# Optimization experiments

Hardware: AMD Instinct MI355X
Metric: run time of the kernel (lower is better)

The kernel has to match this reference:

```python
import jax, jax.numpy as jnp
import numpy as np

N_HEAD = 12
SCALING = 0.17677669529663687  # 1/sqrt(head_dim=32)


def setup_inputs() -> dict:
    key = jax.random.key(0)
    ks = jax.random.split(key, 6)
    B, R, C, E = 1, 256, 384, 384
    s = 1.0 / np.sqrt(E)
    return {
        "x": jax.random.normal(ks[0], (B, R, C, E), dtype=jnp.float32),
        "Wq": (jax.random.normal(ks[1], (E, E), dtype=jnp.float32) * s),
        "Wk": (jax.random.normal(ks[2], (E, E), dtype=jnp.float32) * s),
        "Wv": (jax.random.normal(ks[3], (E, E), dtype=jnp.float32) * s),
        "Wq_s": (jax.random.normal(ks[4], (E, E), dtype=jnp.float32) * s),
        "Wk_s": (jax.random.normal(ks[5], (E, E), dtype=jnp.float32) * s),
        "res_mask": jnp.ones((B, C), dtype=jnp.int32),
        "seq_mask": jnp.ones((B, R), dtype=jnp.int32),
    }


def reference(x, Wq, Wk, Wv, Wq_s, Wk_s, res_mask, seq_mask):
    B, R, C, E = x.shape
    H = N_HEAD
    D = E // H
    NEG = jnp.finfo(x.dtype).min

    # ---- SeqWeightAttention: per-column attention over rows, query = row 0 ----
    scale_s = 1.0 / np.sqrt(D)
    msa = jnp.transpose(x, (0, 2, 1, 3))                 # [B,C,R,E]
    q0 = msa[:, :, 0]                                    # [B,C,E]
    Qs = (q0 @ Wq_s).reshape(B, C, 1, H, D)
    Qs = jnp.transpose(Qs, (0, 1, 3, 2, 4)) * scale_s    # [B,C,H,1,D]
    Ks = (msa @ Wk_s).reshape(B, C, R, H, D)
    Ks = jnp.transpose(Ks, (0, 1, 3, 4, 2))              # [B,C,H,D,R]
    QKs = Qs @ Ks                                        # [B,C,H,1,R]
    QKs = jnp.where(seq_mask[:, None, None, None, :] == 0, NEG, QKs)
    sw = jax.nn.softmax(QKs, axis=-1)
    sw = jnp.transpose(sw, (0, 4, 1, 2, 3))              # [B,R,C,H,1]

    # ---- main attention, row-contracted (attn_seq_weight path) ----
    scaling = SCALING / np.sqrt(C)                        # seqlen_scaling=True
    Q = (x @ Wq).reshape(B, R, C, H, D) * scaling * sw    # Q modulated by seq weights
    K = (x @ Wk).reshape(B, R, C, H, D)
    V = (x @ Wv).reshape(B, R, C, H, D)

    QK = jnp.einsum('brihd,brjhd->bhij', Q, K)            # contract rows + head_dim
    rm = res_mask[:, :, None] * res_mask[:, None, :]      # [B,C,C]
    QK = jnp.where(rm[:, None, :, :] == 0, NEG, QK)
    attn = jax.nn.softmax(QK, axis=-1)                    # [B,H,C,C]

    out = jnp.einsum('bhij,brjhd->brihd', attn, V)
    return out.reshape(B, R, C, E)
```

## Files before the change

### kernel.cpp

```cpp
#include <hip/hip_runtime.h>
#include <math.h>
#include <stdint.h>

#define DEV_INLINE __device__ __forceinline__

constexpr int R_ = 256, C_ = 384, E_ = 384, H_ = 12, D_ = 32;
constexpr float NEGF = -3.402823466e38f;

typedef __attribute__((ext_vector_type(4))) float f32x4;
typedef __attribute__((ext_vector_type(8))) short short8;
typedef __attribute__((ext_vector_type(4))) unsigned short u16x4;

constexpr size_t o_qs     = 0;
constexpr size_t o_p      = o_qs + (size_t)C_ * E_;
constexpr size_t o_logits = o_p + (size_t)C_ * H_ * E_;
constexpr size_t o_sw     = o_logits + (size_t)C_ * H_ * R_;
constexpr size_t o_attn   = o_sw + (size_t)C_ * H_ * R_;
constexpr size_t o_q3     = o_attn + (size_t)H_ * C_ * C_;
constexpr size_t SZBIG  = 75497472;
constexpr size_t ob_q3b = o_q3 * 4;
constexpr size_t ob_k3b = ob_q3b + SZBIG;
constexpr size_t ob_v3b = ob_k3b + SZBIG;
constexpr size_t ob_xb  = ob_v3b + SZBIG;

DEV_INLINE unsigned short bf16h(float x) {
  unsigned int u = __builtin_bit_cast(unsigned int, x);
  unsigned int r = (u + 0x7FFFu + ((u >> 16) & 1u)) >> 16;
  return (unsigned short)r;
}
DEV_INLINE float waveRedMax(float v) {
#pragma unroll
  for (int o = 32; o > 0; o >>= 1) v = fmaxf(v, __shfl_down(v, o));
  return v;
}
DEV_INLINE float waveRedSum(float v) {
#pragma unroll
  for (int o = 32; o > 0; o >>= 1) v += __shfl_down(v, o);
  return v;
}

DEV_INLINE void gll16(const void* g, void* l) {
  __builtin_amdgcn_global_load_lds(
      reinterpret_cast<__attribute__((address_space(1))) void*>(
          reinterpret_cast<uintptr_t>(g)),
      reinterpret_cast<__attribute__((address_space(3))) void*>(
          reinterpret_cast<uintptr_t>(l)),
      16, 0, 0);
}

template <int ROWS, int UPR, int MASK, int SHIFT>
DEV_INLINE void stageT(const unsigned short* __restrict__ g, int lda,
                       unsigned short* l) {
  int t = threadIdx.x, w = t >> 6, lane = t & 63;
  constexpr int NI = (ROWS * UPR) / 64;
  constexpr int PW = NI / 4;
#pragma unroll
  for (int j = 0; j < PW; ++j) {
    int u0 = (w * PW + j) * 64;
    int u = u0 + lane;
    int row = u / UPR, qp = u % UPR;
    int q = qp ^ ((row >> SHIFT) & MASK);
    gll16(g + (size_t)row * lda + q * 8, l + (size_t)u0 * 8);
  }
}

template <int MASK, int SHIFT>
DEV_INLINE short8 fragLd(const unsigned short* base, int row, int q, int rowShorts) {
  int qp = q ^ ((row >> SHIFT) & MASK);
  return *(const short8*)(base + row * rowShorts + qp * 8);
}

__global__ void k_qs(const float* __restrict__ x, const float* __restrict__ Wq_s,
                     float* __restrict__ ws) {
  int c = blockIdx.x, t = threadIdx.x;
  __shared__ float xl[E_];
  xl[t] = x[(size_t)c * E_ + t];
  __syncthreads();
  float s = 0.f;
#pragma unroll 8
  for (int k = 0; k < E_; ++k) s += xl[k] * Wq_s[(size_t)k * E_ + t];
  ws[o_qs + (size_t)c * E_ + t] = s * 0.17677669529663687f;
}

__global__ void k_p(const float* __restrict__ Wk_s, const float* __restrict__ ws,
                    unsigned short* __restrict__ Pb) {
  int h = blockIdx.x, c = blockIdx.y, t = threadIdx.x;
  __shared__ float q[D_];
  float s = 0.f;
  if (h < 12) {
    if (t < D_) q[t] = ws[o_qs + (size_t)c * E_ + h * D_ + t];
    __syncthreads();
    const float* wrow = &Wk_s[(size_t)t * E_ + h * D_];
#pragma unroll
    for (int d = 0; d < D_; d += 4) {
      float4 w = *(const float4*)&wrow[d];
      s += w.x * q[d] + w.y * q[d + 1] + w.z * q[d + 2] + w.w * q[d + 3];
    }
  }
  Pb[((size_t)c * 16 + h) * 384 + t] = bf16h(s);
}

__global__ __launch_bounds__(256) void k_logits_sm(
    const unsigned short* __restrict__ xb, const unsigned short* __restrict__ Pb,
    const int* __restrict__ seq_mask, float* __restrict__ swT) {
  int c = blockIdx.x, t = threadIdx.x;
  __shared__ unsigned short sA[256 * 32];
  __shared__ unsigned short sB[16 * 32];
  __shared__ float lg[12 * 256];
  __shared__ float red[4];
  int w = t >> 6, lane = t & 63, id16 = lane & 15, g = lane >> 4;
  f32x4 acc[4];
#pragma unroll
  for (int mi = 0; mi < 4; ++mi) acc[mi] = (f32x4){0.f, 0.f, 0.f, 0.f};

  for (int k0 = 0; k0 < 384; k0 += 32) {
    stageT<256, 4, 3, 0>(xb + (size_t)c * 384 + k0, 384 * 384, sA);
    if (w == 0) {
      int row = lane >> 2, qp = lane & 3, q = qp ^ (row & 3);
      gll16(Pb + ((size_t)c * 16 + row) * 384 + k0 + q * 8, sB);
    }
    __syncthreads();
    short8 Bf = fragLd<3, 0>(sB, id16, g, 32);
#pragma unroll
    for (int mi = 0; mi < 4; ++mi) {
      short8 Af = fragLd<3, 0>(sA, w * 64 + mi * 16 + id16, g, 32);
      acc[mi] = __builtin_amdgcn_mfma_f32_16x16x32_bf16(Af, Bf, acc[mi], 0, 0, 0);
    }
    __syncthreads();
  }
  int l4 = (lane >> 4) * 4;
#pragma unroll
  for (int mi = 0; mi < 4; ++mi) {
    if (id16 < 12) {
      f32x4 a = acc[mi];
#pragma unroll
      for (int reg = 0; reg < 4; ++reg)
        lg[id16 * 256 + w * 64 + mi * 16 + l4 + reg] = a[reg];
    }
  }
  __syncthreads();
  int wid = t >> 6;
  const float scal = 0.17677669529663687f / sqrtf((float)C_);
  bool masked = (seq_mask[t] == 0);
  for (int h = 0; h < 12; ++h) {
    float v = masked ? NEGF : lg[h * 256 + t];
    float m = waveRedMax(v);
    if ((t & 63) == 0) red[wid] = m;
    __syncthreads();
    float mx = fmaxf(fmaxf(red[0], red[1]), fmaxf(red[2], red[3]));
    __syncthreads();
    float e = expf(v - mx);
    float s = waveRedSum(e);
    if ((t & 63) == 0) red[wid] = s;
    __syncthreads();
    float sum = red[0] + red[1] + red[2] + red[3];
    swT[((size_t)h * 256 + t) * 384 + c] = e / sum * scal;
    __syncthreads();
  }
}

__global__ void k_cvt_x(const float* __restrict__ x, unsigned short* __restrict__ xb) {
  size_t i = ((size_t)blockIdx.x * 256 + threadIdx.x) * 16;
  unsigned short h[16];
#pragma unroll
  for (int j = 0; j < 4; ++j) {
    float4 f = *(const float4*)&x[i + j * 4];
    h[j * 4 + 0] = bf16h(f.x);
    h[j * 4 + 1] = bf16h(f.y);
    h[j * 4 + 2] = bf16h(f.z);
    h[j * 4 + 3] = bf16h(f.w);
  }
  *(short8*)&xb[i] = *(const short8*)&h[0];
  *(short8*)&xb[i + 8] = *(const short8*)&h[8];
}

__global__ void k_cvt_w(const float* __restrict__ Wq, const float* __restrict__ Wk,
                        const float* __restrict__ Wv, unsigned short* __restrict__ Wtb) {
  int n = blockIdx.x, k = threadIdx.x;
  const float* W;
  int col;
  if (n < 384)      { W = Wq; col = n; }
  else if (n < 768) { W = Wk; col = n - 384; }
  else              { W = Wv; col = n - 768; }
  Wtb[(size_t)n * 384 + k] = bf16h(W[(size_t)k * 384 + col]);
}

__global__ __launch_bounds__(256, 4) void k_proj_all(
    const unsigned short* __restrict__ xb, const unsigned short* __restrict__ Wtb,
    const float* __restrict__ swT, unsigned short* __restrict__ Q3b,
    unsigned short* __restrict__ K3b, unsigned short* __restrict__ V3b) {
  __shared__ unsigned short smem[2 * 128 * 64];
  unsigned short* sA = smem;
  unsigned short* sB = smem + 128 * 64;
  int Dd = blockIdx.x;
  int L = (Dd & 7) * 864 + (Dd >> 3);
  int bm = L / 9, bn = L - bm * 9;
  int n0 = bn * 128, m0 = bm * 128;
  int wave = threadIdx.x >> 6, wr = wave >> 1, wc = wave & 1;
  int lane = threadIdx.x & 63, id16 = lane & 15, g = lane >> 4;
  f32x4 acc[4][4];
#pragma unroll
  for (int mi = 0; mi < 4; ++mi)
#pragma unroll
    for (int ni = 0; ni < 4; ++ni) acc[mi][ni] = (f32x4){0.f, 0.f, 0.f, 0.f};

  for (int it = 0; it < 6; ++it) {
    stageT<128, 8, 7, 0>(xb + (size_t)m0 * 384 + it * 64, 384, sA);
    stageT<128, 8, 7, 0>(Wtb + (size_t)n0 * 384 + it * 64, 384, sB);
    __syncthreads();
    short8 Af[4][2], Bf[4][2];
#pragma unroll
    for (int mi = 0; mi < 4; ++mi) {
      int row = wr * 64 + mi * 16 + id16;
#pragma unroll
      for (int kk = 0; kk < 2; ++kk) Af[mi][kk] = fragLd<7, 0>(sA, row, kk * 4 + g, 64);
    }
#pragma unroll
    for (int ni = 0; ni < 4; ++ni) {
      int col = wc * 64 + ni * 16 + id16;
#pragma unroll
      for (int kk = 0; kk < 2; ++kk) Bf[ni][kk] = fragLd<7, 0>(sB, col, kk * 4 + g, 64);
    }
#pragma unroll
    for (int kk = 0; kk < 2; ++kk)
#pragma unroll
      for (int mi = 0; mi < 4; ++mi)
#pragma unroll
        for (int ni = 0; ni < 4; ++ni)
          acc[mi][ni] = __builtin_amdgcn_mfma_f32_16x16x32_bf16(Af[mi][kk], Bf[ni][kk],
                                                                acc[mi][ni], 0, 0, 0);
    __syncthreads();
  }

  int l4 = (lane >> 4) * 4;
  int r = bm / 3, cb = (bm % 3) * 128;
  if (bn < 6) {
    bool isQ = bn < 3;
    int hbase = isQ ? bn * 4 : (bn - 3) * 4;
#pragma unroll
    for (int mi = 0; mi < 4; ++mi) {
      int clBase = wr * 64 + mi * 16 + l4;
#pragma unroll
      for (int ni = 0; ni < 4; ++ni) {
        int nl = wc * 64 + ni * 16 + id16;
        int hhl = nl >> 5, d = nl & 31;
        f32x4 a = acc[mi][ni];
        if (isQ) {
          float4 sv =
              *(const float4*)&swT[((size_t)(hbase + hhl) * 256 + r) * 384 + cb + clBase];
          a[0] *= sv.x; a[1] *= sv.y; a[2] *= sv.z; a[3] *= sv.w;
        }
#pragma unroll
        for (int reg = 0; reg < 4; ++reg)
          smem[hhl * 4096 + (clBase + reg) * 32 + d] = bf16h(a[reg]);
      }
    }
    __syncthreads();
    unsigned short* dst = isQ ? Q3b : K3b;
#pragma unroll
    for (int seg = 0; seg < 8; ++seg) {
      int off = seg * 2048 + threadIdx.x * 8;
      int hhl = off >> 12, inner = off & 4095;
      int hg = hbase + hhl;
      *(short8*)(dst + (((size_t)hg * 256 + r) * 384 + cb) * 32 + inner) =
          *(const short8*)(smem + off);
    }
  } else {
    int r2 = r, cb2 = cb;
#pragma unroll
    for (int mi = 0; mi < 4; ++mi) {
      int c0 = cb2 + wr * 64 + mi * 16 + l4;
#pragma unroll
      for (int ni = 0; ni < 4; ++ni) {
        int nv = n0 + wc * 64 + ni * 16 + id16 - 768;
        int hh = nv >> 5, dd = nv & 31;
        f32x4 a = acc[mi][ni];
        u16x4 hv;
#pragma unroll
        for (int reg = 0; reg < 4; ++reg) hv[reg] = bf16h(a[reg]);
        *(u16x4*)(V3b + ((size_t)hh * 8192 + r2 * 32 + dd) * 384 + c0) = hv;
      }
    }
  }
}

__global__ __launch_bounds__(256, 4) void k_qk_mma(
    const unsigned short* __restrict__ Q3b, const unsigned short* __restrict__ K3b,
    float* __restrict__ QKf0, float* __restrict__ QKf1) {
  __shared__ unsigned short sA[2 * 4096], sB[2 * 4096];
  int Dd = blockIdx.x;
  int L = (Dd & 7) * 27 + (Dd >> 3);
  int kh = L / 108, rem = L - kh * 108;
  int h = rem / 9, r2 = rem - h * 9, bi = r2 / 3, bj = r2 - bi * 3;
  int i0 = bi * 128, j0 = bj * 128;
  int wave = threadIdx.x >> 6, wr = wave >> 1, wc = wave & 1;
  int lane = threadIdx.x & 63, id16 = lane & 15, g = lane >> 4;
  f32x4 acc[4][4];
#pragma unroll
  for (int mi = 0; mi < 4; ++mi)
#pragma unroll
    for (int ni = 0; ni < 4; ++ni) acc[mi][ni] = (f32x4){0.f, 0.f, 0.f, 0.f};

  for (int it = 0; it < 64; ++it) {
    int r = kh * 128 + it * 2;
#pragma unroll
    for (int rr = 0; rr < 2; ++rr) {
      stageT<128, 4, 3, 1>(Q3b + (((size_t)h * 256 + r + rr) * 384 + i0) * 32, 32,
                           sA + rr * 4096);
      stageT<128, 4, 3, 1>(K3b + (((size_t)h * 256 + r + rr) * 384 + j0) * 32, 32,
                           sB + rr * 4096);
    }
    __syncthreads();
#pragma unroll
    for (int rr = 0; rr < 2; ++rr) {
      short8 Af[4], Bf[4];
#pragma unroll
      for (int mi = 0; mi < 4; ++mi)
        Af[mi] = fragLd<3, 1>(sA + rr * 4096, wr * 64 + mi * 16 + id16, g, 32);
#pragma unroll
      for (int ni = 0; ni < 4; ++ni)
        Bf[ni] = fragLd<3, 1>(sB + rr * 4096, wc * 64 + ni * 16 + id16, g, 32);
#pragma unroll
      for (int mi = 0; mi < 4; ++mi)
#pragma unroll
        for (int ni = 0; ni < 4; ++ni)
          acc[mi][ni] = __builtin_amdgcn_mfma_f32_16x16x32_bf16(Af[mi], Bf[ni],
                                                                acc[mi][ni], 0, 0, 0);
    }
    __syncthreads();
  }
  int l4 = (lane >> 4) * 4;
  float* dst = kh ? QKf1 : QKf0;
#pragma unroll
  for (int mi = 0; mi < 4; ++mi)
#pragma unroll
    for (int ni = 0; ni < 4; ++ni) {
      int ii = i0 + wr * 64 + mi * 16 + l4;
      int j = j0 + wc * 64 + ni * 16 + id16;
      f32x4 a = acc[mi][ni];
#pragma unroll
      for (int reg = 0; reg < 4; ++reg)
        dst[((size_t)h * 384 + ii + reg) * 384 + j] = a[reg];
    }
}

__global__ void k_softmax_j(const int* __restrict__ res_mask, const float* __restrict__ QKf0,
                            const float* __restrict__ QKf1,
                            unsigned short* __restrict__ attnb) {
  int i = blockIdx.x, h = blockIdx.y, t = threadIdx.x;
  int lane = t & 63, wid = t >> 6;
  size_t base = ((size_t)h * C_ + i) * C_;
  float v = QKf0[base + t] + QKf1[base + t];
  if ((res_mask[i] * res_mask[t]) == 0) v = NEGF;
  __shared__ float red[6];
  float m = waveRedMax(v);
  if (lane == 0) red[wid] = m;
  __syncthreads();
  float mx = red[0];
#pragma unroll
  for (int w = 1; w < 6; ++w) mx = fmaxf(mx, red[w]);
  __syncthreads();
  float e = expf(v - mx);
  float s = waveRedSum(e);
  if (lane == 0) red[wid] = s;
  __syncthreads();
  float sum = 0.f;
#pragma unroll
  for (int w = 0; w < 6; ++w) sum += red[w];
  attnb[base + t] = bf16h(e / sum);
}

__global__ __launch_bounds__(256, 4) void k_out_mma(
    const unsigned short* __restrict__ attnb, const unsigned short* __restrict__ V3b,
    float* __restrict__ out) {
  __shared__ unsigned short sA[128 * 64], sB[128 * 64];
  int Dd = blockIdx.x;
  int L = (Dd & 7) * 288 + (Dd >> 3);
  int bn = L % 64, bm = (L / 64) % 3, h = L / 192;
  int n0 = bn * 128, m0 = bm * 128;
  int wave = threadIdx.x >> 6, wr = wave >> 1, wc = wave & 1;
  int lane = threadIdx.x & 63, id16 = lane & 15, g = lane >> 4;
  f32x4 acc[4][4];
#pragma unroll
  for (int mi = 0; mi < 4; ++mi)
#pragma unroll
    for (int ni = 0; ni < 4; ++ni) acc[mi][ni] = (f32x4){0.f, 0.f, 0.f, 0.f};
  const unsigned short* Ab = attnb + (size_t)h * 384 * 384 + (size_t)m0 * 384;
  const unsigned short* Bb = V3b + (size_t)h * 8192 * 384 + (size_t)n0 * 384;

  for (int it = 0; it < 6; ++it) {
    stageT<128, 8, 7, 0>(Ab + it * 64, 384, sA);
    stageT<128, 8, 7, 0>(Bb + it * 64, 384, sB);
    __syncthreads();
    short8 Af[4][2], Bf[4][2];
#pragma unroll
    for (int mi = 0; mi < 4; ++mi) {
      int row = wr * 64 + mi * 16 + id16;
#pragma unroll
      for (int kk = 0; kk < 2; ++kk) Af[mi][kk] = fragLd<7, 0>(sA, row, kk * 4 + g, 64);
    }
#pragma unroll
    for (int ni = 0; ni < 4; ++ni) {
      int col = wc * 64 + ni * 16 + id16;
#pragma unroll
      for (int kk = 0; kk < 2; ++kk) Bf[ni][kk] = fragLd<7, 0>(sB, col, kk * 4 + g, 64);
    }
#pragma unroll
    for (int kk = 0; kk < 2; ++kk)
#pragma unroll
      for (int mi = 0; mi < 4; ++mi)
#pragma unroll
        for (int ni = 0; ni < 4; ++ni)
          acc[mi][ni] = __builtin_amdgcn_mfma_f32_16x16x32_bf16(Af[mi][kk], Bf[ni][kk],
                                                                acc[mi][ni], 0, 0, 0);
    __syncthreads();
  }
  int l4 = (lane >> 4) * 4;
#pragma unroll
  for (int mi = 0; mi < 4; ++mi)
#pragma unroll
    for (int ni = 0; ni < 4; ++ni) {
      int i0 = m0 + wr * 64 + mi * 16 + l4;
      int n = n0 + wc * 64 + ni * 16 + id16;
      int r = n >> 5, d = n & 31;
      f32x4 a = acc[mi][ni];
#pragma unroll
      for (int reg = 0; reg < 4; ++reg)
        out[(((size_t)r * 384 + i0 + reg) * 12 + h) * 32 + d] = a[reg];
    }
}

extern "C" void kernel_launch(void* const* d_in, const int* in_sizes, int n_in,
                              void* d_out, int out_size, void* d_ws, size_t ws_size,
                              hipStream_t stream) {
  const float* x = (const float*)d_in[0];
  const float* Wq = (const float*)d_in[1];
  const float* Wk = (const float*)d_in[2];
  const float* Wv = (const float*)d_in[3];
  const float* Wq_s = (const float*)d_in[4];
  const float* Wk_s = (const float*)d_in[5];
  const int* res_mask = (const int*)d_in[6];
  const int* seq_mask = (const int*)d_in[7];
  float* ws = (float*)d_ws;
  char* wsb = (char*)d_ws;
  float* out = (float*)d_out;

  unsigned short* Pb  = (unsigned short*)(wsb + o_p * 4);
  float* swT          = ws + o_logits;
  unsigned short* Wtb = (unsigned short*)(wsb + o_attn * 4);
  float* QKf0         = ws + o_attn;
  unsigned short* Q3b = (unsigned short*)(wsb + ob_q3b);
  unsigned short* K3b = (unsigned short*)(wsb + ob_k3b);
  unsigned short* V3b = (unsigned short*)(wsb + ob_v3b);
  unsigned short* xb  = (unsigned short*)(wsb + ob_xb);
  unsigned short* attnb = Q3b;
  float* QKf1 = (float*)(wsb + ob_xb);

  hipLaunchKernelGGL(k_cvt_x, dim3(9216), dim3(256), 0, stream, x, xb);
  hipLaunchKernelGGL(k_qs, dim3(C_), dim3(E_), 0, stream, x, Wq_s, ws);
  hipLaunchKernelGGL(k_p, dim3(16, C_), dim3(E_), 0, stream, Wk_s, ws, Pb);
  hipLaunchKernelGGL(k_logits_sm, dim3(C_), dim3(256), 0, stream, xb, Pb, seq_mask, swT);
  hipLaunchKernelGGL(k_cvt_w, dim3(1152), dim3(384), 0, stream, Wq, Wk, Wv, Wtb);
  hipLaunchKernelGGL(k_proj_all, dim3(6912), dim3(256), 0, stream, xb, Wtb, swT,
                     Q3b, K3b, V3b);
  hipLaunchKernelGGL(k_qk_mma, dim3(216), dim3(256), 0, stream, Q3b, K3b, QKf0, QKf1);
  hipLaunchKernelGGL(k_softmax_j, dim3(C_, H_), dim3(C_), 0, stream, res_mask,
                     QKf0, QKf1, attnb);
  hipLaunchKernelGGL(k_out_mma, dim3(2304), dim3(256), 0, stream, attnb, V3b, out);
}
```

Before: 399.5 us.

## Split QK row reduction four ways and stage output stores through LDS

The QK^T reduction over rows is split into four partial sums instead of two, doubling the grid to 432 blocks so more CUs are busy on the 256-CU part. The softmax then sums four fp32 partial buffers, which adds extra workspace traffic. The out_mma epilogue now transposes accumulators through shared memory so each thread writes float4-coalesced rows of the output instead of scattered scalar stores. This adds extra syncs and LDS traffic in the epilogue.

```diff
diff --git a/kernel.cpp b/kernel.cpp
--- a/kernel.cpp
+++ b/kernel.cpp
@@ -22,6 +22,7 @@
 constexpr size_t ob_k3b = ob_q3b + SZBIG;
 constexpr size_t ob_v3b = ob_k3b + SZBIG;
 constexpr size_t ob_xb  = ob_v3b + SZBIG;
+constexpr size_t QKSZ   = 7077888;
 
 DEV_INLINE unsigned short bf16h(float x) {
   unsigned int u = __builtin_bit_cast(unsigned int, x);
@@ -189,7 +190,7 @@
     const unsigned short* __restrict__ xb, const unsigned short* __restrict__ Wtb,
     const float* __restrict__ swT, unsigned short* __restrict__ Q3b,
     unsigned short* __restrict__ K3b, unsigned short* __restrict__ V3b) {
-  __shared__ unsigned short smem[2 * 128 * 64];
+  __shared__ __align__(16) unsigned short smem[2 * 128 * 64];
   unsigned short* sA = smem;
   unsigned short* sB = smem + 128 * 64;
   int Dd = blockIdx.x;
@@ -266,10 +267,9 @@
           *(const short8*)(smem + off);
     }
   } else {
-    int r2 = r, cb2 = cb;
-#pragma unroll
-    for (int mi = 0; mi < 4; ++mi) {
-      int c0 = cb2 + wr * 64 + mi * 16 + l4;
+#pragma unroll
+    for (int mi = 0; mi < 4; ++mi) {
+      int c0 = cb + wr * 64 + mi * 16 + l4;
 #pragma unroll
       for (int ni = 0; ni < 4; ++ni) {
         int nv = n0 + wc * 64 + ni * 16 + id16 - 768;
@@ -278,7 +278,7 @@
         u16x4 hv;
 #pragma unroll
         for (int reg = 0; reg < 4; ++reg) hv[reg] = bf16h(a[reg]);
-        *(u16x4*)(V3b + ((size_t)hh * 8192 + r2 * 32 + dd) * 384 + c0) = hv;
+        *(u16x4*)(V3b + ((size_t)hh * 8192 + r * 32 + dd) * 384 + c0) = hv;
       }
     }
   }
@@ -286,10 +286,11 @@
 
 __global__ __launch_bounds__(256, 4) void k_qk_mma(
     const unsigned short* __restrict__ Q3b, const unsigned short* __restrict__ K3b,
-    float* __restrict__ QKf0, float* __restrict__ QKf1) {
+    float* __restrict__ QKf0, float* __restrict__ QKf1,
+    float* __restrict__ QKf2, float* __restrict__ QKf3) {
   __shared__ unsigned short sA[2 * 4096], sB[2 * 4096];
   int Dd = blockIdx.x;
-  int L = (Dd & 7) * 27 + (Dd >> 3);
+  int L = (Dd & 7) * 54 + (Dd >> 3);
   int kh = L / 108, rem = L - kh * 108;
   int h = rem / 9, r2 = rem - h * 9, bi = r2 / 3, bj = r2 - bi * 3;
   int i0 = bi * 128, j0 = bj * 128;
@@ -301,8 +302,8 @@
 #pragma unroll
     for (int ni = 0; ni < 4; ++ni) acc[mi][ni] = (f32x4){0.f, 0.f, 0.f, 0.f};
 
-  for (int it = 0; it < 64; ++it) {
-    int r = kh * 128 + it * 2;
+  for (int it = 0; it < 32; ++it) {
+    int r = kh * 64 + it * 2;
 #pragma unroll
     for (int rr = 0; rr < 2; ++rr) {
       stageT<128, 4, 3, 1>(Q3b + (((size_t)h * 256 + r + rr) * 384 + i0) * 32, 32,
@@ -330,7 +331,7 @@
     __syncthreads();
   }
   int l4 = (lane >> 4) * 4;
-  float* dst = kh ? QKf1 : QKf0;
+  float* dst = (kh == 0) ? QKf0 : (kh == 1) ? QKf1 : (kh == 2) ? QKf2 : QKf3;
 #pragma unroll
   for (int mi = 0; mi < 4; ++mi)
 #pragma unroll
@@ -345,12 +346,13 @@
 }
 
 __global__ void k_softmax_j(const int* __restrict__ res_mask, const float* __restrict__ QKf0,
-                            const float* __restrict__ QKf1,
+                            const float* __restrict__ QKf1, const float* __restrict__ QKf2,
+                            const float* __restrict__ QKf3,
                             unsigned short* __restrict__ attnb) {
   int i = blockIdx.x, h = blockIdx.y, t = threadIdx.x;
   int lane = t & 63, wid = t >> 6;
   size_t base = ((size_t)h * C_ + i) * C_;
-  float v = QKf0[base + t] + QKf1[base + t];
+  float v = (QKf0[base + t] + QKf1[base + t]) + (QKf2[base + t] + QKf3[base + t]);
   if ((res_mask[i] * res_mask[t]) == 0) v = NEGF;
   __shared__ float red[6];
   float m = waveRedMax(v);
@@ -373,7 +375,9 @@
 __global__ __launch_bounds__(256, 4) void k_out_mma(
     const unsigned short* __restrict__ attnb, const unsigned short* __restrict__ V3b,
     float* __restrict__ out) {
-  __shared__ unsigned short sA[128 * 64], sB[128 * 64];
+  __shared__ __align__(16) unsigned short smem[2 * 128 * 64];
+  unsigned short* sA = smem;
+  unsigned short* sB = smem + 128 * 64;
   int Dd = blockIdx.x;
   int L = (Dd & 7) * 288 + (Dd >> 3);
   int bn = L % 64, bm = (L / 64) % 3, h = L / 192;
@@ -415,19 +419,36 @@
                                                                 acc[mi][ni], 0, 0, 0);
     __syncthreads();
   }
+
   int l4 = (lane >> 4) * 4;
-#pragma unroll
-  for (int mi = 0; mi < 4; ++mi)
-#pragma unroll
-    for (int ni = 0; ni < 4; ++ni) {
-      int i0 = m0 + wr * 64 + mi * 16 + l4;
-      int n = n0 + wc * 64 + ni * 16 + id16;
-      int r = n >> 5, d = n & 31;
-      f32x4 a = acc[mi][ni];
-#pragma unroll
-      for (int reg = 0; reg < 4; ++reg)
-        out[(((size_t)r * 384 + i0 + reg) * 12 + h) * 32 + d] = a[reg];
-    }
+  float* smf = (float*)smem;
+#pragma unroll
+  for (int p = 0; p < 2; ++p) {
+#pragma unroll
+    for (int mi = 0; mi < 4; ++mi) {
+      int iL = wr * 64 + mi * 16 + l4;
+#pragma unroll
+      for (int nq = 0; nq < 2; ++nq) {
+        int ni = 2 * p + nq;
+        int d = nq * 16 + id16;
+        f32x4 a = acc[mi][ni];
+#pragma unroll
+        for (int reg = 0; reg < 4; ++reg)
+          smf[wc * 4096 + (iL + reg) * 32 + d] = a[reg];
+      }
+    }
+    __syncthreads();
+#pragma unroll
+    for (int seg = 0; seg < 8; ++seg) {
+      int o = seg * 1024 + threadIdx.x * 4;
+      int plane = o >> 12, rest = o & 4095;
+      int iL = rest >> 5, d = rest & 31;
+      int rg = (n0 >> 5) + plane * 2 + p;
+      *(float4*)&out[(((size_t)rg * 384 + m0 + iL) * 12 + h) * 32 + d] =
+          *(const float4*)&smf[o];
+    }
+    __syncthreads();
+  }
 }
 
 extern "C" void kernel_launch(void* const* d_in, const int* in_sizes, int n_in,
@@ -455,6 +476,8 @@
   unsigned short* xb  = (unsigned short*)(wsb + ob_xb);
   unsigned short* attnb = Q3b;
   float* QKf1 = (float*)(wsb + ob_xb);
+  float* QKf2 = (float*)(wsb + ob_xb + QKSZ);
+  float* QKf3 = (float*)(wsb + ob_xb + 2 * QKSZ);
 
   hipLaunchKernelGGL(k_cvt_x, dim3(9216), dim3(256), 0, stream, x, xb);
   hipLaunchKernelGGL(k_qs, dim3(C_), dim3(E_), 0, stream, x, Wq_s, ws);
@@ -463,8 +486,9 @@
   hipLaunchKernelGGL(k_cvt_w, dim3(1152), dim3(384), 0, stream, Wq, Wk, Wv, Wtb);
   hipLaunchKernelGGL(k_proj_all, dim3(6912), dim3(256), 0, stream, xb, Wtb, swT,
                      Q3b, K3b, V3b);
-  hipLaunchKernelGGL(k_qk_mma, dim3(216), dim3(256), 0, stream, Q3b, K3b, QKf0, QKf1);
+  hipLaunchKernelGGL(k_qk_mma, dim3(432), dim3(256), 0, stream, Q3b, K3b,
+                     QKf0, QKf1, QKf2, QKf3);
   hipLaunchKernelGGL(k_softmax_j, dim3(C_, H_), dim3(C_), 0, stream, res_mask,
-                     QKf0, QKf1, attnb);
+                     QKf0, QKf1, QKf2, QKf3, attnb);
   hipLaunchKernelGGL(k_out_mma, dim3(2304), dim3(256), 0, stream, attnb, V3b, out);
 }
```

After: 373.1 us. -6.6%, faster.
